# Performance work log

Hardware: AMD Instinct MI355X
Metric: run time of the kernel (lower is better)

Reference implementation:

```python
import jax, jax.numpy as jnp
import numpy as np

B, IN_F, N_HID = 2048, 512, 2048
HEAD = N_HID + IN_F  # 2560


def setup_inputs() -> dict:
    key = jax.random.key(0)
    ks = jax.random.split(key, 14)
    scale = 1.0 / np.sqrt(HEAD)
    # sparsity mask: original [IN_F, N_HID] in {-1,0,1}; _prep_mask pads with
    # ones [N_HID, N_HID], transposes, abs -> [N_HID, HEAD] of {0,1}
    raw = jax.random.randint(ks[0], (IN_F, N_HID), -1, 2).astype(jnp.float32)
    mask = jnp.abs(jnp.concatenate([raw, jnp.ones((N_HID, N_HID), jnp.float32)], axis=0).T)
    def w(k):
        return jax.random.normal(k, (N_HID, HEAD), jnp.float32) * scale
    def b(k):
        return jax.random.normal(k, (N_HID,), jnp.float32) * scale
    return {
        "x": jax.random.normal(ks[1], (B, IN_F), jnp.float32),
        "hidden": jax.random.normal(ks[2], (B, N_HID), jnp.float32),
        "mask": mask,
        "Wg": w(ks[3]), "bg": b(ks[4]),
        "Wh": w(ks[5]), "bh": b(ks[6]),
        "Wfg": w(ks[7]), "bfg": b(ks[8]),
        "Wfh": w(ks[9]), "bfh": b(ks[10]),
        "Wp": w(ks[11]), "bp": b(ks[12]),
    }


def reference(x, hidden, mask, Wg, bg, Wh, bh, Wfg, bfg, Wfh, bfh, Wp, bp):
    # concatenated input shared by all 5 masked linears: [B, HEAD]
    xc = jnp.concatenate([x, hidden], axis=1)
    # fuse the 5 masked GEMMs into one: [5, N_HID, HEAD] stacked weights
    W_all = jnp.stack([Wg, Wh, Wfg, Wfh, Wp]) * mask[None]
    b_all = jnp.stack([bg, bh, bfg, bfh, bp])
    outs = jnp.einsum('bh,koh->kbo', xc, W_all) + b_all[:, None, :]  # [5, B, N_HID]
    g_out, h_out, fg_out, fh_out, p_out = outs
    g = jnp.tanh(g_out)
    h = jnp.tanh(h_out)
    gate = jax.nn.sigmoid(fg_out + fh_out)
    new_hidden = g * (1.0 - gate) + gate * h
    y_pred = p_out + new_hidden
    return (y_pred, new_hidden)
```

## Files before the change

### kernel.cpp

```cpp
#include <hip/hip_runtime.h>

#define MDIM 2048
#define KD   2560
#define NHID 2048
#define INF  512
#define NTOT 10240
#define NS   40

typedef __attribute__((ext_vector_type(4))) float f32x4;
typedef __attribute__((ext_vector_type(8))) short short8;
typedef __attribute__((ext_vector_type(8))) unsigned short ushort8v;
typedef __attribute__((ext_vector_type(4))) unsigned short ushort4v;

#define AS1 __attribute__((address_space(1)))
#define AS3 __attribute__((address_space(3)))

__device__ __forceinline__ unsigned short f2bf(float f) {
    unsigned u = __float_as_uint(f);
    u += 0x7fffu + ((u >> 16) & 1u);
    return (unsigned short)(u >> 16);
}
__device__ __forceinline__ float bf2f(unsigned short s) {
    return __uint_as_float(((unsigned)s) << 16);
}

__global__ void prep_xc(const float* __restrict__ x, const float* __restrict__ h,
                        unsigned short* __restrict__ xc) {
    int idx = blockIdx.x * 256 + threadIdx.x;
    int e = idx * 8;
    int b = e / KD;
    int c = e - b * KD;
    const float* src = (c < INF) ? (x + (size_t)b * INF + c)
                                 : (h + (size_t)b * NHID + (c - INF));
    float4 v0 = *(const float4*)src;
    float4 v1 = *(const float4*)(src + 4);
    ushort8v o;
    o[0] = f2bf(v0.x); o[1] = f2bf(v0.y); o[2] = f2bf(v0.z); o[3] = f2bf(v0.w);
    o[4] = f2bf(v1.x); o[5] = f2bf(v1.y); o[6] = f2bf(v1.z); o[7] = f2bf(v1.w);
    *(ushort8v*)(xc + e) = o;
}

__global__ void prep_wm(const float* __restrict__ Wg, const float* __restrict__ Wh,
                        const float* __restrict__ Wfg, const float* __restrict__ Wfh,
                        const float* __restrict__ Wp, const float* __restrict__ mask,
                        unsigned short* __restrict__ Wm) {
    int idx = blockIdx.x * 256 + threadIdx.x;
    size_t e = (size_t)idx * 4;
    const size_t PL = (size_t)NHID * KD;
    float4 m = *(const float4*)(mask + e);
    const float* Ws[5] = {Wg, Wh, Wfg, Wfh, Wp};
    #pragma unroll
    for (int k = 0; k < 5; ++k) {
        float4 w = *(const float4*)(Ws[k] + e);
        ushort4v o;
        o[0] = f2bf(w.x * m.x); o[1] = f2bf(w.y * m.y);
        o[2] = f2bf(w.z * m.z); o[3] = f2bf(w.w * m.w);
        *(ushort4v*)(Wm + k * PL + e) = o;
    }
}

#define MFMA(d, va, vb) d = __builtin_amdgcn_mfma_f32_16x16x32_bf16(va, vb, d, 0, 0, 0)

__global__ __launch_bounds__(512, 2) void gemm8p(
    const unsigned short* __restrict__ A,
    const unsigned short* __restrict__ B,
    unsigned short* __restrict__ C) {
    __shared__ unsigned short lsA[2][256 * 64];
    __shared__ unsigned short lsB[2][320 * 64];

    const int tid  = threadIdx.x;
    const int lane = tid & 63;
    const int w    = tid >> 6;
    const int wm   = w >> 2;
    const int wn   = w & 3;
    const int lr   = lane & 15;
    const int kq   = lane >> 4;
    const int l7   = lane & 7;
    const int m0   = blockIdx.y * 256;
    const int n0   = blockIdx.x * 320;

    const unsigned short* gA = A + (size_t)m0 * KD;
    const unsigned short* gB = B + (size_t)n0 * KD;
    const int soff = (lane >> 3) * KD + (((lane & 7) ^ (lane >> 3)) << 3);

    const int ar0 = (w >> 2) * 128 + (w & 3) * 8;
    const int br0 = (w >> 1) * 80 + (w & 1) * 8;

#define SA(j, t, b) __builtin_amdgcn_global_load_lds( \
        (const AS1 unsigned int*)(gA + (size_t)(ar0 + 32 * (j)) * KD + (t) * 64 + soff), \
        (AS3 unsigned int*)(&lsA[b][(ar0 + 32 * (j)) * 64]), 16, 0, 0)
#define SB(j, t, b) __builtin_amdgcn_global_load_lds( \
        (const AS1 unsigned int*)(gB + (size_t)(br0 + ((j) < 2 ? 16 * (j) : 32 + 16 * ((j) - 2))) * KD + (t) * 64 + soff), \
        (AS3 unsigned int*)(&lsB[b][(br0 + ((j) < 2 ? 16 * (j) : 32 + 16 * ((j) - 2))) * 64]), 16, 0, 0)

    const int c0 = ((0 + kq) ^ l7) << 3;
    const int c1 = ((4 + kq) ^ l7) << 3;
    const int arow = wm * 128 + lr;
    const int brow = wn * 80 + lr;

#define LDA(dst, b, m, cs) dst = *(const short8*)&lsA[b][(arow + 16 * (m)) * 64 + (cs)]
#define LDB(dst, b, n, cs) dst = *(const short8*)&lsB[b][(brow + 16 * (n)) * 64 + (cs)]

#define FBAR() do { asm volatile("" ::: "memory"); __builtin_amdgcn_s_barrier(); asm volatile("" ::: "memory"); } while (0)
#define VBAR() do { asm volatile("s_waitcnt vmcnt(9)" ::: "memory"); __builtin_amdgcn_s_barrier(); asm volatile("" ::: "memory"); } while (0)

    f32x4 acc[8][5] = {};

    SA(0, 0, 0); SA(1, 0, 0); SB(0, 0, 0); SB(1, 0, 0);
    SA(2, 0, 0); SA(3, 0, 0); SB(2, 0, 0); SB(3, 0, 0); SB(4, 0, 0);
    SA(0, 1, 1); SA(1, 1, 1); SB(0, 1, 1); SB(1, 1, 1);
    VBAR();

    for (int kt = 0; kt < NS; ++kt) {
        const int bc = kt & 1, bo = bc ^ 1;
        short8 fa[4][2], fb[2][2], fc[3][2];

        #pragma unroll
        for (int m = 0; m < 4; ++m) { LDA(fa[m][0], bc, m, c0); LDA(fa[m][1], bc, m, c1); }
        #pragma unroll
        for (int n = 0; n < 2; ++n) { LDB(fb[n][0], bc, n, c0); LDB(fb[n][1], bc, n, c1); }
        if (kt < NS - 1) { SA(2, kt + 1, bo); SA(3, kt + 1, bo); SB(2, kt + 1, bo); SB(3, kt + 1, bo); SB(4, kt + 1, bo); }
        FBAR();
        __builtin_amdgcn_s_setprio(1);
        #pragma unroll
        for (int m = 0; m < 4; ++m)
            #pragma unroll
            for (int n = 0; n < 2; ++n) { MFMA(acc[m][n], fa[m][0], fb[n][0]); MFMA(acc[m][n], fa[m][1], fb[n][1]); }
        __builtin_amdgcn_s_setprio(0);
        VBAR();

        #pragma unroll
        for (int j = 0; j < 3; ++j) { LDB(fc[j][0], bc, 2 + j, c0); LDB(fc[j][1], bc, 2 + j, c1); }
        FBAR();
        __builtin_amdgcn_s_setprio(1);
        #pragma unroll
        for (int m = 0; m < 4; ++m)
            #pragma unroll
            for (int j = 0; j < 3; ++j) { MFMA(acc[m][2 + j], fa[m][0], fc[j][0]); MFMA(acc[m][2 + j], fa[m][1], fc[j][1]); }
        __builtin_amdgcn_s_setprio(0);
        FBAR();

        #pragma unroll
        for (int m = 0; m < 4; ++m) { LDA(fa[m][0], bc, 4 + m, c0); LDA(fa[m][1], bc, 4 + m, c1); }
        #pragma unroll
        for (int n = 0; n < 2; ++n) { LDB(fb[n][0], bc, n, c0); LDB(fb[n][1], bc, n, c1); }
        if (kt < NS - 2) { SA(0, kt + 2, bc); SA(1, kt + 2, bc); }
        FBAR();
        __builtin_amdgcn_s_setprio(1);
        #pragma unroll
        for (int m = 0; m < 4; ++m)
            #pragma unroll
            for (int n = 0; n < 2; ++n) { MFMA(acc[4 + m][n], fa[m][0], fb[n][0]); MFMA(acc[4 + m][n], fa[m][1], fb[n][1]); }
        __builtin_amdgcn_s_setprio(0);
        FBAR();

        #pragma unroll
        for (int j = 0; j < 3; ++j) { LDB(fc[j][0], bc, 2 + j, c0); LDB(fc[j][1], bc, 2 + j, c1); }
        if (kt < NS - 2) { SB(0, kt + 2, bc); SB(1, kt + 2, bc); }
        FBAR();
        __builtin_amdgcn_s_setprio(1);
        #pragma unroll
        for (int m = 0; m < 4; ++m)
            #pragma unroll
            for (int j = 0; j < 3; ++j) { MFMA(acc[4 + m][2 + j], fa[m][0], fc[j][0]); MFMA(acc[4 + m][2 + j], fa[m][1], fc[j][1]); }
        __builtin_amdgcn_s_setprio(0);
        VBAR();
    }

    #pragma unroll
    for (int m = 0; m < 8; ++m) {
        int row = m0 + wm * 128 + m * 16 + kq * 4;
        #pragma unroll
        for (int n = 0; n < 5; ++n) {
            int col = n0 + wn * 80 + n * 16 + lr;
            #pragma unroll
            for (int j = 0; j < 4; ++j)
                C[(size_t)(row + j) * NTOT + col] = f2bf(acc[m][n][j]);
        }
    }
#undef SA
#undef SB
#undef LDA
#undef LDB
#undef FBAR
#undef VBAR
}

__global__ void epilogue(const unsigned short* __restrict__ C,
                         const float* __restrict__ bg, const float* __restrict__ bh,
                         const float* __restrict__ bfg, const float* __restrict__ bfh,
                         const float* __restrict__ bp,
                         float* __restrict__ out) {
    int idx = blockIdx.x * 256 + threadIdx.x;
    size_t e = (size_t)idx * 8;
    int b = (int)(e >> 11);
    int o = (int)(e & (NHID - 1));
    const size_t PL = (size_t)MDIM * NHID;
    const unsigned short* row = C + (size_t)b * NTOT + o;

    ushort8v vg  = *(const ushort8v*)(row + 0 * NHID);
    ushort8v vh  = *(const ushort8v*)(row + 1 * NHID);
    ushort8v vfg = *(const ushort8v*)(row + 2 * NHID);
    ushort8v vfh = *(const ushort8v*)(row + 3 * NHID);
    ushort8v vp  = *(const ushort8v*)(row + 4 * NHID);

    float bgv[8], bhv[8], bfgv[8], bfhv[8], bpv[8];
    *(float4*)bgv  = *(const float4*)(bg + o);  *(float4*)(bgv + 4)  = *(const float4*)(bg + o + 4);
    *(float4*)bhv  = *(const float4*)(bh + o);  *(float4*)(bhv + 4)  = *(const float4*)(bh + o + 4);
    *(float4*)bfgv = *(const float4*)(bfg + o); *(float4*)(bfgv + 4) = *(const float4*)(bfg + o + 4);
    *(float4*)bfhv = *(const float4*)(bfh + o); *(float4*)(bfhv + 4) = *(const float4*)(bfh + o + 4);
    *(float4*)bpv  = *(const float4*)(bp + o);  *(float4*)(bpv + 4)  = *(const float4*)(bp + o + 4);

    float yv[8], nhv[8];
    #pragma unroll
    for (int j = 0; j < 8; ++j) {
        float g    = tanhf(bf2f(vg[j]) + bgv[j]);
        float hh   = tanhf(bf2f(vh[j]) + bhv[j]);
        float s    = bf2f(vfg[j]) + bfgv[j] + bf2f(vfh[j]) + bfhv[j];
        float gate = 1.0f / (1.0f + __expf(-s));
        float nh   = g * (1.0f - gate) + gate * hh;
        nhv[j] = nh;
        yv[j]  = bf2f(vp[j]) + bpv[j] + nh;
    }
    *(float4*)(out + e)          = *(float4*)yv;
    *(float4*)(out + e + 4)      = *(float4*)(yv + 4);
    *(float4*)(out + PL + e)     = *(float4*)nhv;
    *(float4*)(out + PL + e + 4) = *(float4*)(nhv + 4);
}

extern "C" void kernel_launch(void* const* d_in, const int* in_sizes, int n_in,
                              void* d_out, int out_size, void* d_ws, size_t ws_size,
                              hipStream_t stream) {
    const float* x      = (const float*)d_in[0];
    const float* hidden = (const float*)d_in[1];
    const float* mask   = (const float*)d_in[2];
    const float* Wg     = (const float*)d_in[3];
    const float* bg     = (const float*)d_in[4];
    const float* Wh     = (const float*)d_in[5];
    const float* bh     = (const float*)d_in[6];
    const float* Wfg    = (const float*)d_in[7];
    const float* bfg    = (const float*)d_in[8];
    const float* Wfh    = (const float*)d_in[9];
    const float* bfh    = (const float*)d_in[10];
    const float* Wp     = (const float*)d_in[11];
    const float* bp     = (const float*)d_in[12];
    float* out = (float*)d_out;

    const size_t need = (size_t)MDIM * KD * 2 + (size_t)NTOT * KD * 2
                      + (size_t)MDIM * NTOT * 2;
    if (ws_size < need) return;

    unsigned short* xc = (unsigned short*)d_ws;
    unsigned short* Wm = xc + (size_t)MDIM * KD;
    unsigned short* C  = Wm + (size_t)NTOT * KD;

    prep_xc<<<MDIM * KD / 8 / 256, 256, 0, stream>>>(x, hidden, xc);
    prep_wm<<<NHID * KD / 4 / 256, 256, 0, stream>>>(Wg, Wh, Wfg, Wfh, Wp, mask, Wm);
    dim3 grid(NTOT / 320, MDIM / 256);
    gemm8p<<<grid, 512, 0, stream>>>(xc, Wm, C);
    epilogue<<<MDIM * NHID / 8 / 256, 256, 0, stream>>>(C, bg, bh, bfg, bfh, bp, out);
}
```

Before: 154.4 us.

## Switch GEMM to 32x32x16 MFMA with simpler double-buffered pipeline

Replaces the 16x16x32 bf16 MFMA tiling with 32x32x16 MFMAs. The 8 waves are rearranged into a 4x2 layout, each wave computing 64x160 with 2x5 accumulators of 16 floats. The old four-phase, eight-barrier interleaved pipeline becomes a single prefetch of the next k-tile per iteration, followed by a full vmcnt(0) wait and one barrier. The larger MFMA tile is meant to cut LDS reads per FLOP and the instruction count. The risk is losing the fine-grained overlap of global-to-LDS loads with compute, and a possibly different LDS bank-conflict pattern for the new read layout.

```diff
diff --git a/kernel.cpp b/kernel.cpp
--- a/kernel.cpp
+++ b/kernel.cpp
@@ -7,7 +7,7 @@
 #define NTOT 10240
 #define NS   40
 
-typedef __attribute__((ext_vector_type(4))) float f32x4;
+typedef __attribute__((ext_vector_type(16))) float f32x16;
 typedef __attribute__((ext_vector_type(8))) short short8;
 typedef __attribute__((ext_vector_type(8))) unsigned short ushort8v;
 typedef __attribute__((ext_vector_type(4))) unsigned short ushort4v;
@@ -59,9 +59,9 @@
     }
 }
 
-#define MFMA(d, va, vb) d = __builtin_amdgcn_mfma_f32_16x16x32_bf16(va, vb, d, 0, 0, 0)
-
-__global__ __launch_bounds__(512, 2) void gemm8p(
+#define MFMA32(d, va, vb) d = __builtin_amdgcn_mfma_f32_32x32x16_bf16(va, vb, d, 0, 0, 0)
+
+__global__ __launch_bounds__(512, 2) void gemm32(
     const unsigned short* __restrict__ A,
     const unsigned short* __restrict__ B,
     unsigned short* __restrict__ C) {
@@ -71,10 +71,10 @@
     const int tid  = threadIdx.x;
     const int lane = tid & 63;
     const int w    = tid >> 6;
-    const int wm   = w >> 2;
-    const int wn   = w & 3;
-    const int lr   = lane & 15;
-    const int kq   = lane >> 4;
+    const int wm   = w >> 1;
+    const int wn   = w & 1;
+    const int l31  = lane & 31;
+    const int hi   = lane >> 5;
     const int l7   = lane & 7;
     const int m0   = blockIdx.y * 256;
     const int n0   = blockIdx.x * 320;
@@ -82,7 +82,6 @@
     const unsigned short* gA = A + (size_t)m0 * KD;
     const unsigned short* gB = B + (size_t)n0 * KD;
     const int soff = (lane >> 3) * KD + (((lane & 7) ^ (lane >> 3)) << 3);
-
     const int ar0 = (w >> 2) * 128 + (w & 3) * 8;
     const int br0 = (w >> 1) * 80 + (w & 1) * 8;
 
@@ -90,100 +89,63 @@
         (const AS1 unsigned int*)(gA + (size_t)(ar0 + 32 * (j)) * KD + (t) * 64 + soff), \
         (AS3 unsigned int*)(&lsA[b][(ar0 + 32 * (j)) * 64]), 16, 0, 0)
 #define SB(j, t, b) __builtin_amdgcn_global_load_lds( \
-        (const AS1 unsigned int*)(gB + (size_t)(br0 + ((j) < 2 ? 16 * (j) : 32 + 16 * ((j) - 2))) * KD + (t) * 64 + soff), \
-        (AS3 unsigned int*)(&lsB[b][(br0 + ((j) < 2 ? 16 * (j) : 32 + 16 * ((j) - 2))) * 64]), 16, 0, 0)
-
-    const int c0 = ((0 + kq) ^ l7) << 3;
-    const int c1 = ((4 + kq) ^ l7) << 3;
-    const int arow = wm * 128 + lr;
-    const int brow = wn * 80 + lr;
-
-#define LDA(dst, b, m, cs) dst = *(const short8*)&lsA[b][(arow + 16 * (m)) * 64 + (cs)]
-#define LDB(dst, b, n, cs) dst = *(const short8*)&lsB[b][(brow + 16 * (n)) * 64 + (cs)]
-
-#define FBAR() do { asm volatile("" ::: "memory"); __builtin_amdgcn_s_barrier(); asm volatile("" ::: "memory"); } while (0)
-#define VBAR() do { asm volatile("s_waitcnt vmcnt(9)" ::: "memory"); __builtin_amdgcn_s_barrier(); asm volatile("" ::: "memory"); } while (0)
-
-    f32x4 acc[8][5] = {};
-
-    SA(0, 0, 0); SA(1, 0, 0); SB(0, 0, 0); SB(1, 0, 0);
-    SA(2, 0, 0); SA(3, 0, 0); SB(2, 0, 0); SB(3, 0, 0); SB(4, 0, 0);
-    SA(0, 1, 1); SA(1, 1, 1); SB(0, 1, 1); SB(1, 1, 1);
-    VBAR();
+        (const AS1 unsigned int*)(gB + (size_t)(br0 + 16 * (j)) * KD + (t) * 64 + soff), \
+        (AS3 unsigned int*)(&lsB[b][(br0 + 16 * (j)) * 64]), 16, 0, 0)
+
+    const int arow = wm * 64 + l31;
+    const int brow = wn * 160 + l31;
+
+    f32x16 acc[2][5] = {};
+
+    SA(0, 0, 0); SA(1, 0, 0); SA(2, 0, 0); SA(3, 0, 0);
+    SB(0, 0, 0); SB(1, 0, 0); SB(2, 0, 0); SB(3, 0, 0); SB(4, 0, 0);
+    asm volatile("s_waitcnt vmcnt(0)" ::: "memory");
+    __builtin_amdgcn_s_barrier();
 
     for (int kt = 0; kt < NS; ++kt) {
         const int bc = kt & 1, bo = bc ^ 1;
-        short8 fa[4][2], fb[2][2], fc[3][2];
-
+        if (kt < NS - 1) {
+            SA(0, kt + 1, bo); SA(1, kt + 1, bo); SA(2, kt + 1, bo); SA(3, kt + 1, bo);
+            SB(0, kt + 1, bo); SB(1, kt + 1, bo); SB(2, kt + 1, bo); SB(3, kt + 1, bo); SB(4, kt + 1, bo);
+        }
         #pragma unroll
-        for (int m = 0; m < 4; ++m) { LDA(fa[m][0], bc, m, c0); LDA(fa[m][1], bc, m, c1); }
-        #pragma unroll
-        for (int n = 0; n < 2; ++n) { LDB(fb[n][0], bc, n, c0); LDB(fb[n][1], bc, n, c1); }
-        if (kt < NS - 1) { SA(2, kt + 1, bo); SA(3, kt + 1, bo); SB(2, kt + 1, bo); SB(3, kt + 1, bo); SB(4, kt + 1, bo); }
-        FBAR();
-        __builtin_amdgcn_s_setprio(1);
-        #pragma unroll
-        for (int m = 0; m < 4; ++m)
-            #pragma unroll
-            for (int n = 0; n < 2; ++n) { MFMA(acc[m][n], fa[m][0], fb[n][0]); MFMA(acc[m][n], fa[m][1], fb[n][1]); }
-        __builtin_amdgcn_s_setprio(0);
-        VBAR();
-
-        #pragma unroll
-        for (int j = 0; j < 3; ++j) { LDB(fc[j][0], bc, 2 + j, c0); LDB(fc[j][1], bc, 2 + j, c1); }
-        FBAR();
-        __builtin_amdgcn_s_setprio(1);
-        #pragma unroll
-        for (int m = 0; m < 4; ++m)
-            #pragma unroll
-            for (int j = 0; j < 3; ++j) { MFMA(acc[m][2 + j], fa[m][0], fc[j][0]); MFMA(acc[m][2 + j], fa[m][1], fc[j][1]); }
-        __builtin_amdgcn_s_setprio(0);
-        FBAR();
-
-        #pragma unroll
-        for (int m = 0; m < 4; ++m) { LDA(fa[m][0], bc, 4 + m, c0); LDA(fa[m][1], bc, 4 + m, c1); }
-        #pragma unroll
-        for (int n = 0; n < 2; ++n) { LDB(fb[n][0], bc, n, c0); LDB(fb[n][1], bc, n, c1); }
-        if (kt < NS - 2) { SA(0, kt + 2, bc); SA(1, kt + 2, bc); }
-        FBAR();
-        __builtin_amdgcn_s_setprio(1);
-        #pragma unroll
-        for (int m = 0; m < 4; ++m)
-            #pragma unroll
-            for (int n = 0; n < 2; ++n) { MFMA(acc[4 + m][n], fa[m][0], fb[n][0]); MFMA(acc[4 + m][n], fa[m][1], fb[n][1]); }
-        __builtin_amdgcn_s_setprio(0);
-        FBAR();
-
-        #pragma unroll
-        for (int j = 0; j < 3; ++j) { LDB(fc[j][0], bc, 2 + j, c0); LDB(fc[j][1], bc, 2 + j, c1); }
-        if (kt < NS - 2) { SB(0, kt + 2, bc); SB(1, kt + 2, bc); }
-        FBAR();
-        __builtin_amdgcn_s_setprio(1);
-        #pragma unroll
-        for (int m = 0; m < 4; ++m)
-            #pragma unroll
-            for (int j = 0; j < 3; ++j) { MFMA(acc[4 + m][2 + j], fa[m][0], fc[j][0]); MFMA(acc[4 + m][2 + j], fa[m][1], fc[j][1]); }
-        __builtin_amdgcn_s_setprio(0);
-        VBAR();
+        for (int s = 0; s < 4; ++s) {
+            const int cs = (((2 * s + hi) ^ l7) << 3);
+            short8 av[2], bv[5];
+            #pragma unroll
+            for (int m = 0; m < 2; ++m)
+                av[m] = *(const short8*)&lsA[bc][(arow + 32 * m) * 64 + cs];
+            #pragma unroll
+            for (int n = 0; n < 5; ++n)
+                bv[n] = *(const short8*)&lsB[bc][(brow + 32 * n) * 64 + cs];
+            __builtin_amdgcn_s_setprio(1);
+            #pragma unroll
+            for (int m = 0; m < 2; ++m)
+                #pragma unroll
+                for (int n = 0; n < 5; ++n)
+                    MFMA32(acc[m][n], av[m], bv[n]);
+            __builtin_amdgcn_s_setprio(0);
+        }
+        asm volatile("s_waitcnt vmcnt(0)" ::: "memory");
+        __builtin_amdgcn_s_barrier();
     }
 
     #pragma unroll
-    for (int m = 0; m < 8; ++m) {
-        int row = m0 + wm * 128 + m * 16 + kq * 4;
+    for (int m = 0; m < 2; ++m) {
         #pragma unroll
         for (int n = 0; n < 5; ++n) {
-            int col = n0 + wn * 80 + n * 16 + lr;
-            #pragma unroll
-            for (int j = 0; j < 4; ++j)
-                C[(size_t)(row + j) * NTOT + col] = f2bf(acc[m][n][j]);
+            int col = n0 + wn * 160 + n * 32 + l31;
+            #pragma unroll
+            for (int q = 0; q < 4; ++q) {
+                int row = m0 + wm * 64 + m * 32 + q * 8 + 4 * hi;
+                #pragma unroll
+                for (int t = 0; t < 4; ++t)
+                    C[(size_t)(row + t) * NTOT + col] = f2bf(acc[m][n][q * 4 + t]);
+            }
         }
     }
 #undef SA
 #undef SB
-#undef LDA
-#undef LDB
-#undef FBAR
-#undef VBAR
 }
 
 __global__ void epilogue(const unsigned short* __restrict__ C,
@@ -257,6 +219,6 @@
     prep_xc<<<MDIM * KD / 8 / 256, 256, 0, stream>>>(x, hidden, xc);
     prep_wm<<<NHID * KD / 4 / 256, 256, 0, stream>>>(Wg, Wh, Wfg, Wfh, Wp, mask, Wm);
     dim3 grid(NTOT / 320, MDIM / 256);
-    gemm8p<<<grid, 512, 0, stream>>>(xc, Wm, C);
+    gemm32<<<grid, 512, 0, stream>>>(xc, Wm, C);
     epilogue<<<MDIM * NHID / 8 / 256, 256, 0, stream>>>(C, bg, bh, bfg, bfh, bp, out);
 }
```

Measured after the change: 156.1 us. Within noise of the previous version (+1.1%).
